# Kernel optimization log

Hardware: AMD Instinct MI355X
Metric: run time of the kernel (lower is better)

Reference implementation:

```python
import jax, jax.numpy as jnp
import numpy as np

N, D, K = 65536, 1024, 256

def setup_inputs() -> dict:
    key = jax.random.key(0)
    k1, k2 = jax.random.split(key)
    inputs = jax.random.normal(k1, (N, D), dtype=jnp.float32)
    centroids = jax.random.normal(k2, (K, D), dtype=jnp.float32)
    return {"inputs": inputs, "centroids": centroids}

def reference(inputs, centroids):
    # Squared euclidean distances [K, N] without materializing [K, N, D]:
    # ||c||^2 + ||x||^2 - 2 c @ x^T  (same math as sum(square(x[None]-c[:,None]), -1))
    x_sq = jnp.sum(inputs * inputs, axis=1)            # [N]
    c_sq = jnp.sum(centroids * centroids, axis=1)      # [K]
    cross = jnp.einsum('kd,nd->kn', centroids, inputs) # [K, N]
    distances = c_sq[:, None] + x_sq[None, :] - 2.0 * cross  # [K, N]
    assignments = jnp.argmin(distances, axis=0)        # [N], int
    # calculate_loss: sum_c mean(where(assign==c, distances, 0)) over the full
    # [K,N] grid. Since each n matches exactly one cluster c, the per-cluster
    # masked means sum to the global mean of distances.
    loss = jnp.mean(distances)
    return distances, assignments, loss
```

## Files before the change

kernel.cpp:

```cpp
#include <hip/hip_runtime.h>
#include <cstdint>

#define N_PTS 65536
#define DIM   1024
#define K_CL  256
#define BN    256
#define BK    32
#define NT    (DIM / BK)
#define THREADS 512

typedef __bf16 bf16_t;
typedef bf16_t bf16x8 __attribute__((ext_vector_type(8)));
typedef float  f32x4  __attribute__((ext_vector_type(4)));

union U16x8 { uint4 u4; bf16x8 bf; ushort us[8]; };

__device__ __forceinline__ ushort f2bf_rne(float f) {
    uint32_t u = __float_as_uint(f);
    uint32_t r = (u + 0x7FFFu + ((u >> 16) & 1u)) >> 16;
    return (ushort)r;
}
__device__ __forceinline__ float bf2f(ushort b) {
    return __uint_as_float(((uint32_t)b) << 16);
}

__device__ __forceinline__ void gll16(const void* g, void* l) {
    __builtin_amdgcn_global_load_lds(
        (const __attribute__((address_space(1))) void*)g,
        (__attribute__((address_space(3))) void*)l, 16, 0, 0);
}

#define BAR()   __builtin_amdgcn_s_barrier()
#define SCHB()  __builtin_amdgcn_sched_barrier(0)
#define LGKM0() do { asm volatile("s_waitcnt lgkmcnt(0)" ::: "memory"); \
                     __builtin_amdgcn_sched_barrier(0); } while (0)
#define VMCNT(N) do { asm volatile("s_waitcnt vmcnt(" #N ")" ::: "memory"); \
                      __builtin_amdgcn_sched_barrier(0); } while (0)
#define MFMA(ACC, A, B) (ACC) = __builtin_amdgcn_mfma_f32_16x16x32_bf16((A).bf, (B).bf, (ACC), 0, 0, 0)

__global__ __launch_bounds__(128) void km_prep(const float* __restrict__ cent,
                                               ushort* __restrict__ Ahi,
                                               ushort* __restrict__ Alo,
                                               float* __restrict__ csq) {
    const int r  = blockIdx.x;
    const int j  = threadIdx.x;
    const int kt = j >> 2;
    const int gp = j & 3;
    const int s  = (r >> 1) & 3;
    const int d0 = kt * BK + ((gp ^ s) << 3);

    const float* src = cent + r * DIM + d0;
    float4 a = *(const float4*)src;
    float4 b = *(const float4*)(src + 4);
    float v[8] = {a.x, a.y, a.z, a.w, b.x, b.y, b.z, b.w};

    U16x8 hi, lo;
    float ss = 0.f;
#pragma unroll
    for (int i = 0; i < 8; ++i) {
        float f = v[i];
        ss += f * f;
        ushort h = f2bf_rne(f);
        hi.us[i] = h;
        lo.us[i] = f2bf_rne(f - bf2f(h));
    }
    *(uint4*)(Ahi + kt * (K_CL * BK) + r * BK + gp * 8) = hi.u4;
    *(uint4*)(Alo + kt * (K_CL * BK) + r * BK + gp * 8) = lo.u4;

#pragma unroll
    for (int off = 1; off < 64; off <<= 1) ss += __shfl_xor(ss, off);
    __shared__ float ws2[2];
    if ((j & 63) == 0) ws2[j >> 6] = ss;
    __syncthreads();
    if (j == 0) csq[r] = ws2[0] + ws2[1];
}

__global__ __launch_bounds__(THREADS, 2) void km_main(
    const float* __restrict__ x,
    const ushort* __restrict__ Ahi, const ushort* __restrict__ Alo,
    const float* __restrict__ csq,
    float* __restrict__ out_dist, float* __restrict__ out_assign,
    float* __restrict__ partials) {

    __shared__ __align__(16) ushort sAhi[2][K_CL * BK];
    __shared__ __align__(16) ushort sAlo[2][K_CL * BK];
    __shared__ __align__(16) ushort sBhi[2][BN * BK];
    __shared__ __align__(16) ushort sBlo[2][BN * BK];
    __shared__ __align__(16) float  sCsq[K_CL];
    __shared__ __align__(16) float  sXsq[BN];
    __shared__ float sRedV[4 * BN];
    __shared__ int   sRedI[4 * BN];
    __shared__ float sWsum[8];

    const int tid  = threadIdx.x;
    const int blk  = blockIdx.x;
    const int lane = tid & 63;
    const int w    = tid >> 6;
    const int wr   = w >> 1;
    const int wc   = w & 1;
    const int l15  = lane & 15;
    const int l4   = lane >> 4;

    if (tid < K_CL) sCsq[tid] = csq[tid];

    const int bcol  = tid >> 1;
    const int bhalf = tid & 1;
    const int bs    = (bcol >> 1) & 3;
    const int bOff0 = bcol * BK + ((((bhalf << 1) | 0) ^ bs) << 3);
    const int bOff1 = bcol * BK + ((((bhalf << 1) | 1) ^ bs) << 3);
    const float* xsrc = x + (size_t)(blk * BN + bcol) * DIM + bhalf * 16;

    float xs_acc = 0.f;

    auto stageA = [&](int kt, int buf) {
        const char* ph = (const char*)Ahi + kt * 16384 + tid * 16;
        const char* pl = (const char*)Alo + kt * 16384 + tid * 16;
        char* dh = (char*)&sAhi[buf][0] + tid * 16;
        char* dl = (char*)&sAlo[buf][0] + tid * 16;
        gll16(ph,        dh);
        gll16(ph + 8192, dh + 8192);
        gll16(pl,        dl);
        gll16(pl + 8192, dl + 8192);
    };
    auto writeB = [&](int buf, float4 v0, float4 v1, float4 v2, float4 v3) {
        float f[16] = {v0.x, v0.y, v0.z, v0.w, v1.x, v1.y, v1.z, v1.w,
                       v2.x, v2.y, v2.z, v2.w, v3.x, v3.y, v3.z, v3.w};
        U16x8 h0, h1, l0, l1;
#pragma unroll
        for (int i = 0; i < 8; ++i) {
            float a = f[i];
            xs_acc = fmaf(a, a, xs_acc);
            bf16_t hb = (bf16_t)a;
            h0.bf[i] = hb;
            l0.bf[i] = (bf16_t)(a - (float)hb);
            float b = f[i + 8];
            xs_acc = fmaf(b, b, xs_acc);
            bf16_t hc = (bf16_t)b;
            h1.bf[i] = hc;
            l1.bf[i] = (bf16_t)(b - (float)hc);
        }
        *(uint4*)&sBhi[buf][bOff0] = h0.u4;
        *(uint4*)&sBhi[buf][bOff1] = h1.u4;
        *(uint4*)&sBlo[buf][bOff0] = l0.u4;
        *(uint4*)&sBlo[buf][bOff1] = l1.u4;
    };

    int aOff[4], bOff[8];
#pragma unroll
    for (int f = 0; f < 4; ++f) {
        int row  = wr * 64 + f * 16 + l15;
        aOff[f]  = row * BK + ((l4 ^ ((row >> 1) & 3)) << 3);
    }
#pragma unroll
    for (int f = 0; f < 8; ++f) {
        int col  = wc * 128 + f * 16 + l15;
        bOff[f]  = col * BK + ((l4 ^ ((col >> 1) & 3)) << 3);
    }

    float4 b0, b1, b2, b3;
    stageA(0, 0);
    b0 = *(const float4*)(xsrc);
    b1 = *(const float4*)(xsrc + 4);
    b2 = *(const float4*)(xsrc + 8);
    b3 = *(const float4*)(xsrc + 12);
    writeB(0, b0, b1, b2, b3);
    {
        const float* p = xsrc + BK;
        b0 = *(const float4*)p;
        b1 = *(const float4*)(p + 4);
        b2 = *(const float4*)(p + 8);
        b3 = *(const float4*)(p + 12);
    }
    __syncthreads();

    f32x4 acc[4][8];
#pragma unroll
    for (int i = 0; i < 4; ++i)
#pragma unroll
        for (int q = 0; q < 8; ++q) acc[i][q] = (f32x4){0.f, 0.f, 0.f, 0.f};

    for (int kt = 0; kt < NT; ++kt) {
        const int  cur = kt & 1, nxt = cur ^ 1;
        const bool pf1 = (kt + 1 < NT);
        const bool pf2 = (kt + 2 < NT);

        U16x8 ah[4], al[4];
#pragma unroll
        for (int f = 0; f < 4; ++f) {
            ah[f].u4 = *(const uint4*)&sAhi[cur][aOff[f]];
            al[f].u4 = *(const uint4*)&sAlo[cur][aOff[f]];
        }

        if (pf1) stageA(kt + 1, nxt);
        SCHB();
        if (pf1) writeB(nxt, b0, b1, b2, b3);
        SCHB();
        if (pf2) {
            const float* p = xsrc + (kt + 2) * BK;
            b0 = *(const float4*)p;
            b1 = *(const float4*)(p + 4);
            b2 = *(const float4*)(p + 8);
            b3 = *(const float4*)(p + 12);
        }
        SCHB();

        __builtin_amdgcn_s_setprio(1);
#pragma unroll
        for (int fj = 0; fj < 8; ++fj) {
            U16x8 bh, bl;
            bh.u4 = *(const uint4*)&sBhi[cur][bOff[fj]];
            bl.u4 = *(const uint4*)&sBlo[cur][bOff[fj]];
#pragma unroll
            for (int fi = 0; fi < 4; ++fi) MFMA(acc[fi][fj], ah[fi], bh);
#pragma unroll
            for (int fi = 0; fi < 4; ++fi) MFMA(acc[fi][fj], ah[fi], bl);
#pragma unroll
            for (int fi = 0; fi < 4; ++fi) MFMA(acc[fi][fj], al[fi], bh);
        }
        __builtin_amdgcn_s_setprio(0);

        if (pf2)      { VMCNT(4); }
        else if (pf1) { VMCNT(0); }
        LGKM0();
        BAR();
    }

    {
        float v = xs_acc;
        v += __shfl_xor(v, 1);
        if (bhalf == 0) sXsq[bcol] = v;
    }
    __syncthreads();

    const int colBase = wc * 128;
    float xs[8];
    f32x4 cs[4];
#pragma unroll
    for (int f = 0; f < 8; ++f) xs[f] = sXsq[colBase + f * 16 + l15];
#pragma unroll
    for (int f = 0; f < 4; ++f) cs[f] = *(const f32x4*)&sCsq[wr * 64 + f * 16 + l4 * 4];

    float lsum = 0.f;
    float bestv[8];
    int   bestr[8];
#pragma unroll
    for (int f = 0; f < 8; ++f) { bestv[f] = 3.4e38f; bestr[f] = 0; }

#pragma unroll
    for (int fi = 0; fi < 4; ++fi) {
        const int rowB = wr * 64 + fi * 16 + l4 * 4;
#pragma unroll
        for (int fj = 0; fj < 8; ++fj) {
            const int col = blk * BN + colBase + fj * 16 + l15;
            float* outp = out_dist + (size_t)rowB * N_PTS + col;
#pragma unroll
            for (int j = 0; j < 4; ++j) {
                float d = cs[fi][j] + xs[fj] - 2.0f * acc[fi][fj][j];
                outp[(size_t)j * N_PTS] = d;
                lsum += d;
                int r = rowB + j;
                if (d < bestv[fj]) { bestv[fj] = d; bestr[fj] = r; }
            }
        }
    }

#pragma unroll
    for (int fj = 0; fj < 8; ++fj) {
#pragma unroll
        for (int m = 16; m <= 32; m <<= 1) {
            float ov = __shfl_xor(bestv[fj], m);
            int   orr = __shfl_xor(bestr[fj], m);
            if (ov < bestv[fj] || (ov == bestv[fj] && orr < bestr[fj])) {
                bestv[fj] = ov; bestr[fj] = orr;
            }
        }
        if (lane < 16) {
            sRedV[wr * BN + colBase + fj * 16 + lane] = bestv[fj];
            sRedI[wr * BN + colBase + fj * 16 + lane] = bestr[fj];
        }
    }

#pragma unroll
    for (int off = 1; off < 64; off <<= 1) lsum += __shfl_xor(lsum, off);
    if (lane == 0) sWsum[w] = lsum;
    __syncthreads();

    if (tid < BN) {
        float bv = sRedV[tid];
        int   br = sRedI[tid];
#pragma unroll
        for (int q = 1; q < 4; ++q) {
            float v = sRedV[q * BN + tid];
            int   r = sRedI[q * BN + tid];
            if (v < bv || (v == bv && r < br)) { bv = v; br = r; }
        }
        out_assign[blk * BN + tid] = (float)br;
    }
    if (tid == 0) {
        float t = 0.f;
#pragma unroll
        for (int q = 0; q < 8; ++q) t += sWsum[q];
        partials[blk] = t;
    }
}

__global__ __launch_bounds__(256) void km_fin(const float* __restrict__ partials,
                                              float* __restrict__ out_loss) {
    __shared__ float ws[4];
    const int t = threadIdx.x;
    float v = partials[t];
#pragma unroll
    for (int off = 1; off < 64; off <<= 1) v += __shfl_xor(v, off);
    if ((t & 63) == 0) ws[t >> 6] = v;
    __syncthreads();
    if (t == 0) {
        float s = 0.f;
#pragma unroll
        for (int i = 0; i < 4; ++i) s += ws[i];
        out_loss[0] = s / 16777216.0f;
    }
}

extern "C" void kernel_launch(void* const* d_in, const int* in_sizes, int n_in,
                              void* d_out, int out_size, void* d_ws, size_t ws_size,
                              hipStream_t stream) {
    const float* x    = (const float*)d_in[0];
    const float* cent = (const float*)d_in[1];

    float* out        = (float*)d_out;
    float* out_dist   = out;
    float* out_assign = out + (size_t)K_CL * N_PTS;
    float* out_loss   = out_assign + N_PTS;

    char*   ws       = (char*)d_ws;
    float*  csq      = (float*)ws;
    float*  partials = (float*)(ws + 1024);
    ushort* Ahi      = (ushort*)(ws + 4096);
    ushort* Alo      = (ushort*)(ws + 4096 + 524288);

    km_prep<<<dim3(K_CL), dim3(128), 0, stream>>>(cent, Ahi, Alo, csq);
    km_main<<<dim3(N_PTS / BN), dim3(THREADS), 0, stream>>>(
        x, Ahi, Alo, csq, out_dist, out_assign, partials);
    km_fin<<<dim3(1), dim3(256), 0, stream>>>(partials, out_loss);
}
```

Baseline: 118.3 us.

## Halve point tile to 128, double K-step to 64, single-buffer centroid tile

Shrinks the per-block point tile from 256 to 128 columns, so twice as many blocks run, and processes 64 dimensions per iteration as two 32-wide sub-steps, halving the loop trip count. The centroid tile in shared memory becomes single-buffered over the wider K-step, with an extra barrier after reading it into registers. Only half the threads stage and convert x. The final reduction kernel grows to 512 threads to match the larger number of partial sums. This trades fewer barriers and more blocks for lower MFMA reuse per block, since each block now re-reads the full centroid set for half as many points. The A prefetch also loses overlap with compute.

```diff
diff --git a/kernel.cpp b/kernel.cpp
--- a/kernel.cpp
+++ b/kernel.cpp
@@ -4,9 +4,9 @@
 #define N_PTS 65536
 #define DIM   1024
 #define K_CL  256
-#define BN    256
+#define BN    128
 #define BK    32
-#define NT    (DIM / BK)
+#define NKT   16
 #define THREADS 512
 
 typedef __bf16 bf16_t;
@@ -84,8 +84,8 @@
 
     __shared__ __align__(16) ushort sAhi[2][K_CL * BK];
     __shared__ __align__(16) ushort sAlo[2][K_CL * BK];
-    __shared__ __align__(16) ushort sBhi[2][BN * BK];
-    __shared__ __align__(16) ushort sBlo[2][BN * BK];
+    __shared__ __align__(16) ushort sBhi[2][2][BN * BK];
+    __shared__ __align__(16) ushort sBlo[2][2][BN * BK];
     __shared__ __align__(16) float  sCsq[K_CL];
     __shared__ __align__(16) float  sXsq[BN];
     __shared__ float sRedV[4 * BN];
@@ -100,6 +100,7 @@
     const int wc   = w & 1;
     const int l15  = lane & 15;
     const int l4   = lane >> 4;
+    const bool stager = (tid < 256);
 
     if (tid < K_CL) sCsq[tid] = csq[tid];
 
@@ -108,21 +109,25 @@
     const int bs    = (bcol >> 1) & 3;
     const int bOff0 = bcol * BK + ((((bhalf << 1) | 0) ^ bs) << 3);
     const int bOff1 = bcol * BK + ((((bhalf << 1) | 1) ^ bs) << 3);
-    const float* xsrc = x + (size_t)(blk * BN + bcol) * DIM + bhalf * 16;
+    const float* xsrc = x + (size_t)(blk * BN + (bcol & 127)) * DIM + bhalf * 16;
 
     float xs_acc = 0.f;
 
-    auto stageA = [&](int kt, int buf) {
-        const char* ph = (const char*)Ahi + kt * 16384 + tid * 16;
-        const char* pl = (const char*)Alo + kt * 16384 + tid * 16;
-        char* dh = (char*)&sAhi[buf][0] + tid * 16;
-        char* dl = (char*)&sAlo[buf][0] + tid * 16;
-        gll16(ph,        dh);
-        gll16(ph + 8192, dh + 8192);
-        gll16(pl,        dl);
-        gll16(pl + 8192, dl + 8192);
+    auto stageA = [&](int kt64) {
+        const char* ph = (const char*)Ahi + (size_t)kt64 * 32768 + tid * 16;
+        const char* pl = (const char*)Alo + (size_t)kt64 * 32768 + tid * 16;
+        char* dh = (char*)&sAhi[0][0] + tid * 16;
+        char* dl = (char*)&sAlo[0][0] + tid * 16;
+        gll16(ph,         dh);
+        gll16(ph +  8192, dh +  8192);
+        gll16(ph + 16384, dh + 16384);
+        gll16(ph + 24576, dh + 24576);
+        gll16(pl,         dl);
+        gll16(pl +  8192, dl +  8192);
+        gll16(pl + 16384, dl + 16384);
+        gll16(pl + 24576, dl + 24576);
     };
-    auto writeB = [&](int buf, float4 v0, float4 v1, float4 v2, float4 v3) {
+    auto writeB = [&](int buf, int ks, float4 v0, float4 v1, float4 v2, float4 v3) {
         float f[16] = {v0.x, v0.y, v0.z, v0.w, v1.x, v1.y, v1.z, v1.w,
                        v2.x, v2.y, v2.z, v2.w, v3.x, v3.y, v3.z, v3.w};
         U16x8 h0, h1, l0, l1;
@@ -139,118 +144,133 @@
             h1.bf[i] = hc;
             l1.bf[i] = (bf16_t)(b - (float)hc);
         }
-        *(uint4*)&sBhi[buf][bOff0] = h0.u4;
-        *(uint4*)&sBhi[buf][bOff1] = h1.u4;
-        *(uint4*)&sBlo[buf][bOff0] = l0.u4;
-        *(uint4*)&sBlo[buf][bOff1] = l1.u4;
+        *(uint4*)&sBhi[buf][ks][bOff0] = h0.u4;
+        *(uint4*)&sBhi[buf][ks][bOff1] = h1.u4;
+        *(uint4*)&sBlo[buf][ks][bOff0] = l0.u4;
+        *(uint4*)&sBlo[buf][ks][bOff1] = l1.u4;
     };
 
-    int aOff[4], bOff[8];
+    int aOff[4], bOff[4];
 #pragma unroll
     for (int f = 0; f < 4; ++f) {
         int row  = wr * 64 + f * 16 + l15;
         aOff[f]  = row * BK + ((l4 ^ ((row >> 1) & 3)) << 3);
-    }
-#pragma unroll
-    for (int f = 0; f < 8; ++f) {
-        int col  = wc * 128 + f * 16 + l15;
+        int col  = wc * 64 + f * 16 + l15;
         bOff[f]  = col * BK + ((l4 ^ ((col >> 1) & 3)) << 3);
     }
 
-    float4 b0, b1, b2, b3;
-    stageA(0, 0);
-    b0 = *(const float4*)(xsrc);
-    b1 = *(const float4*)(xsrc + 4);
-    b2 = *(const float4*)(xsrc + 8);
-    b3 = *(const float4*)(xsrc + 12);
-    writeB(0, b0, b1, b2, b3);
-    {
-        const float* p = xsrc + BK;
-        b0 = *(const float4*)p;
-        b1 = *(const float4*)(p + 4);
-        b2 = *(const float4*)(p + 8);
-        b3 = *(const float4*)(p + 12);
-    }
-    __syncthreads();
-
-    f32x4 acc[4][8];
+    float4 pA0, pA1, pA2, pA3, pB0, pB1, pB2, pB3;
+    stageA(0);
+    if (stager) {
+        pA0 = *(const float4*)(xsrc);
+        pA1 = *(const float4*)(xsrc + 4);
+        pA2 = *(const float4*)(xsrc + 8);
+        pA3 = *(const float4*)(xsrc + 12);
+        pB0 = *(const float4*)(xsrc + 32);
+        pB1 = *(const float4*)(xsrc + 36);
+        pB2 = *(const float4*)(xsrc + 40);
+        pB3 = *(const float4*)(xsrc + 44);
+        writeB(0, 0, pA0, pA1, pA2, pA3);
+        writeB(0, 1, pB0, pB1, pB2, pB3);
+        const float* p = xsrc + 64;
+        pA0 = *(const float4*)p;       pA1 = *(const float4*)(p + 4);
+        pA2 = *(const float4*)(p + 8); pA3 = *(const float4*)(p + 12);
+        pB0 = *(const float4*)(p + 32); pB1 = *(const float4*)(p + 36);
+        pB2 = *(const float4*)(p + 40); pB3 = *(const float4*)(p + 44);
+    }
+    __syncthreads();
+
+    f32x4 acc[4][4];
 #pragma unroll
     for (int i = 0; i < 4; ++i)
 #pragma unroll
-        for (int q = 0; q < 8; ++q) acc[i][q] = (f32x4){0.f, 0.f, 0.f, 0.f};
-
-    for (int kt = 0; kt < NT; ++kt) {
-        const int  cur = kt & 1, nxt = cur ^ 1;
-        const bool pf1 = (kt + 1 < NT);
-        const bool pf2 = (kt + 2 < NT);
-
-        U16x8 ah[4], al[4];
-#pragma unroll
-        for (int f = 0; f < 4; ++f) {
-            ah[f].u4 = *(const uint4*)&sAhi[cur][aOff[f]];
-            al[f].u4 = *(const uint4*)&sAlo[cur][aOff[f]];
-        }
-
-        if (pf1) stageA(kt + 1, nxt);
-        SCHB();
-        if (pf1) writeB(nxt, b0, b1, b2, b3);
-        SCHB();
-        if (pf2) {
-            const float* p = xsrc + (kt + 2) * BK;
-            b0 = *(const float4*)p;
-            b1 = *(const float4*)(p + 4);
-            b2 = *(const float4*)(p + 8);
-            b3 = *(const float4*)(p + 12);
-        }
-        SCHB();
-
-        __builtin_amdgcn_s_setprio(1);
-#pragma unroll
-        for (int fj = 0; fj < 8; ++fj) {
-            U16x8 bh, bl;
-            bh.u4 = *(const uint4*)&sBhi[cur][bOff[fj]];
-            bl.u4 = *(const uint4*)&sBlo[cur][bOff[fj]];
-#pragma unroll
-            for (int fi = 0; fi < 4; ++fi) MFMA(acc[fi][fj], ah[fi], bh);
-#pragma unroll
-            for (int fi = 0; fi < 4; ++fi) MFMA(acc[fi][fj], ah[fi], bl);
-#pragma unroll
-            for (int fi = 0; fi < 4; ++fi) MFMA(acc[fi][fj], al[fi], bh);
-        }
-        __builtin_amdgcn_s_setprio(0);
-
-        if (pf2)      { VMCNT(4); }
-        else if (pf1) { VMCNT(0); }
+        for (int q = 0; q < 4; ++q) acc[i][q] = (f32x4){0.f, 0.f, 0.f, 0.f};
+
+    int buf = 0;
+    for (int kt = 0; kt < NKT; ++kt) {
+        const bool pf1 = (kt + 1 < NKT);
+        const bool pf2 = (kt + 2 < NKT);
+
+        U16x8 ah[2][4], al[2][4];
+#pragma unroll
+        for (int ks = 0; ks < 2; ++ks)
+#pragma unroll
+            for (int f = 0; f < 4; ++f) {
+                ah[ks][f].u4 = *(const uint4*)&sAhi[ks][aOff[f]];
+                al[ks][f].u4 = *(const uint4*)&sAlo[ks][aOff[f]];
+            }
         LGKM0();
         BAR();
-    }
-
-    {
+
+        if (pf1) stageA(kt + 1);
+        SCHB();
+        if (stager && pf1) {
+            writeB(buf ^ 1, 0, pA0, pA1, pA2, pA3);
+            writeB(buf ^ 1, 1, pB0, pB1, pB2, pB3);
+        }
+        if (stager && pf2) {
+            const float* p = xsrc + (size_t)(kt + 2) * 64;
+            pA0 = *(const float4*)p;        pA1 = *(const float4*)(p + 4);
+            pA2 = *(const float4*)(p + 8);  pA3 = *(const float4*)(p + 12);
+            pB0 = *(const float4*)(p + 32); pB1 = *(const float4*)(p + 36);
+            pB2 = *(const float4*)(p + 40); pB3 = *(const float4*)(p + 44);
+        }
+        SCHB();
+
+        __builtin_amdgcn_s_setprio(1);
+#pragma unroll
+        for (int ks = 0; ks < 2; ++ks) {
+#pragma unroll
+            for (int fj = 0; fj < 4; ++fj) {
+                U16x8 bh, bl;
+                bh.u4 = *(const uint4*)&sBhi[buf][ks][bOff[fj]];
+                bl.u4 = *(const uint4*)&sBlo[buf][ks][bOff[fj]];
+#pragma unroll
+                for (int fi = 0; fi < 4; ++fi) MFMA(acc[fi][fj], ah[ks][fi], bh);
+#pragma unroll
+                for (int fi = 0; fi < 4; ++fi) MFMA(acc[fi][fj], ah[ks][fi], bl);
+#pragma unroll
+                for (int fi = 0; fi < 4; ++fi) MFMA(acc[fi][fj], al[ks][fi], bh);
+            }
+        }
+        __builtin_amdgcn_s_setprio(0);
+
+        if (pf1) {
+            if (stager && pf2) { VMCNT(8); }
+            else              { VMCNT(0); }
+        }
+        LGKM0();
+        BAR();
+        buf ^= 1;
+    }
+
+    if (stager) {
         float v = xs_acc;
         v += __shfl_xor(v, 1);
         if (bhalf == 0) sXsq[bcol] = v;
     }
     __syncthreads();
 
-    const int colBase = wc * 128;
-    float xs[8];
+    const int colBase = wc * 64;
+    float xs[4];
     f32x4 cs[4];
 #pragma unroll
-    for (int f = 0; f < 8; ++f) xs[f] = sXsq[colBase + f * 16 + l15];
-#pragma unroll
-    for (int f = 0; f < 4; ++f) cs[f] = *(const f32x4*)&sCsq[wr * 64 + f * 16 + l4 * 4];
+    for (int f = 0; f < 4; ++f) {
+        xs[f] = sXsq[colBase + f * 16 + l15];
+        cs[f] = *(const f32x4*)&sCsq[wr * 64 + f * 16 + l4 * 4];
+    }
 
     float lsum = 0.f;
-    float bestv[8];
-    int   bestr[8];
-#pragma unroll
-    for (int f = 0; f < 8; ++f) { bestv[f] = 3.4e38f; bestr[f] = 0; }
+    float bestv[4];
+    int   bestr[4];
+#pragma unroll
+    for (int f = 0; f < 4; ++f) { bestv[f] = 3.4e38f; bestr[f] = 0; }
 
 #pragma unroll
     for (int fi = 0; fi < 4; ++fi) {
         const int rowB = wr * 64 + fi * 16 + l4 * 4;
 #pragma unroll
-        for (int fj = 0; fj < 8; ++fj) {
+        for (int fj = 0; fj < 4; ++fj) {
             const int col = blk * BN + colBase + fj * 16 + l15;
             float* outp = out_dist + (size_t)rowB * N_PTS + col;
 #pragma unroll
@@ -265,7 +285,7 @@
     }
 
 #pragma unroll
-    for (int fj = 0; fj < 8; ++fj) {
+    for (int fj = 0; fj < 4; ++fj) {
 #pragma unroll
         for (int m = 16; m <= 32; m <<= 1) {
             float ov = __shfl_xor(bestv[fj], m);
@@ -304,9 +324,9 @@
     }
 }
 
-__global__ __launch_bounds__(256) void km_fin(const float* __restrict__ partials,
+__global__ __launch_bounds__(512) void km_fin(const float* __restrict__ partials,
                                               float* __restrict__ out_loss) {
-    __shared__ float ws[4];
+    __shared__ float ws[8];
     const int t = threadIdx.x;
     float v = partials[t];
 #pragma unroll
@@ -316,7 +336,7 @@
     if (t == 0) {
         float s = 0.f;
 #pragma unroll
-        for (int i = 0; i < 4; ++i) s += ws[i];
+        for (int i = 0; i < 8; ++i) s += ws[i];
         out_loss[0] = s / 16777216.0f;
     }
 }
@@ -341,5 +361,5 @@
     km_prep<<<dim3(K_CL), dim3(128), 0, stream>>>(cent, Ahi, Alo, csq);
     km_main<<<dim3(N_PTS / BN), dim3(THREADS), 0, stream>>>(
         x, Ahi, Alo, csq, out_dist, out_assign, partials);
-    km_fin<<<dim3(1), dim3(256), 0, stream>>>(partials, out_loss);
-}
+    km_fin<<<dim3(1), dim3(512), 0, stream>>>(partials, out_loss);
+}
```

New measurement: 122.3 us. +3.4%, slower.
